# Performance work log

Measured on AMD Instinct MI355X. Metric: run time of the kernel, lower is better.

## Reference

```python
import jax, jax.numpy as jnp
import numpy as np

B, S, D = 2, 2048, 2048
H, H_KV, HD = 8, 1, 256   # attention heads, kv heads, head_dim
N_REP = H // H_KV


def setup_inputs() -> dict:
    key = jax.random.key(0)
    ks = jax.random.split(key, 8)
    std = 1.0 / np.sqrt(D)
    return {
        "hidden_states": jax.random.normal(ks[0], (B, S, D), dtype=jnp.float32),
        "attention_mask": jnp.zeros((B, 1, S, S), dtype=jnp.float32),
        "cos": jax.random.uniform(ks[1], (B, S, HD), dtype=jnp.float32),
        "sin": jax.random.uniform(ks[2], (B, S, HD), dtype=jnp.float32),
        "Wq": jax.random.normal(ks[3], (D, H * HD), dtype=jnp.float32) * std,
        "Wk": jax.random.normal(ks[4], (D, H_KV * HD), dtype=jnp.float32) * std,
        "Wv": jax.random.normal(ks[5], (D, H_KV * HD), dtype=jnp.float32) * std,
        "Wo": jax.random.normal(ks[6], (H * HD, D), dtype=jnp.float32) * std,
    }


def _rotate_half(x):
    x1, x2 = jnp.split(x, 2, axis=-1)
    return jnp.concatenate((-x2, x1), axis=-1)


def reference(hidden_states, attention_mask, cos, sin, Wq, Wk, Wv, Wo):
    b, s, _ = hidden_states.shape
    # projections -> [b, heads, s, hd]
    q = (hidden_states @ Wq).reshape(b, s, H, HD).transpose(0, 2, 1, 3)
    k = (hidden_states @ Wk).reshape(b, s, H_KV, HD).transpose(0, 2, 1, 3)
    v = (hidden_states @ Wv).reshape(b, s, H_KV, HD).transpose(0, 2, 1, 3)
    # RoPE (unsqueeze_dim=1)
    c = cos[:, None, :, :]
    sn = sin[:, None, :, :]
    q = q * c + _rotate_half(q) * sn
    k = k * c + _rotate_half(k) * sn
    # GQA: repeat kv heads
    k = jnp.repeat(k, N_REP, axis=1)
    v = jnp.repeat(v, N_REP, axis=1)
    # attention
    scores = jnp.einsum("bhqd,bhkd->bhqk", q, k) / jnp.sqrt(jnp.float32(HD))
    scores = scores + attention_mask[:, :, :, :k.shape[2]]
    attn_weights = jax.nn.softmax(scores.astype(jnp.float32), axis=-1).astype(q.dtype)
    # dropout p=0.0 -> identity
    out = jnp.einsum("bhqk,bhkd->bhqd", attn_weights, v)
    out = out.transpose(0, 2, 1, 3).reshape(b, s, H * HD)
    out = out @ Wo
    return out, attn_weights
```

## Files before the change

### kernel.cpp

```cpp
#include <hip/hip_runtime.h>
#include <hip/hip_bf16.h>

typedef float f32x4 __attribute__((ext_vector_type(4)));
typedef short short8 __attribute__((ext_vector_type(8)));
typedef unsigned int uint2v __attribute__((ext_vector_type(2)));

#define DI __device__ __forceinline__

DI unsigned short f2bf(float f) {
  unsigned int u = __float_as_uint(f);
  u += 0x7fffu + ((u >> 16) & 1u);
  return (unsigned short)(u >> 16);
}

DI unsigned int packbf(float a, float b) {
  return (unsigned int)f2bf(a) | ((unsigned int)f2bf(b) << 16);
}

DI void gload16(const unsigned short* g, unsigned short* l) {
  __builtin_amdgcn_global_load_lds((const __attribute__((address_space(1))) void*)g,
                                   (__attribute__((address_space(3))) void*)l, 16, 0, 0);
}

__global__ void cvt_bf16_kernel(const float* __restrict__ src,
                                unsigned short* __restrict__ dst, long n) {
  long i = ((long)blockIdx.x * blockDim.x + threadIdx.x) * 8;
  if (i >= n) return;
  float4 a = *(const float4*)(src + i);
  float4 b = *(const float4*)(src + i + 4);
  short8 v;
  v[0] = f2bf(a.x); v[1] = f2bf(a.y); v[2] = f2bf(a.z); v[3] = f2bf(a.w);
  v[4] = f2bf(b.x); v[5] = f2bf(b.y); v[6] = f2bf(b.z); v[7] = f2bf(b.w);
  *(short8*)(dst + i) = v;
}

__global__ void transpose_cvt_kernel(const float* __restrict__ src,
                                     unsigned short* __restrict__ dst,
                                     int ldsrc, int lddst, long sBatch, long dBatch) {
  __shared__ float tile[32][33];
  const float* s = src + (long)blockIdx.z * sBatch;
  unsigned short* d = dst + (long)blockIdx.z * dBatch;
  int c0 = blockIdx.x * 32, r0 = blockIdx.y * 32;
  int tx = threadIdx.x, ty = threadIdx.y;
#pragma unroll
  for (int k = 0; k < 4; k++)
    tile[ty + 8 * k][tx] = s[(long)(r0 + ty + 8 * k) * ldsrc + c0 + tx];
  __syncthreads();
#pragma unroll
  for (int k = 0; k < 4; k++)
    d[(long)(c0 + ty + 8 * k) * lddst + r0 + tx] = f2bf(tile[tx][ty + 8 * k]);
}

__global__ void transpose_v_kernel(const float* __restrict__ qkv,
                                   unsigned short* __restrict__ VtC) {
  __shared__ float tile[32][33];
  int b = blockIdx.z;
  int d0 = blockIdx.x * 32, s0 = blockIdx.y * 32;
  int tx = threadIdx.x, ty = threadIdx.y;
  const float* s = qkv + (long)b * 2048 * 2560 + 2304;
#pragma unroll
  for (int k = 0; k < 4; k++)
    tile[ty + 8 * k][tx] = s[(long)(s0 + ty + 8 * k) * 2560 + d0 + tx];
  __syncthreads();
  unsigned short* d = VtC + (long)b * 524288 + (long)(s0 >> 5) * 8192;
#pragma unroll
  for (int k = 0; k < 4; k++) {
    int dd = d0 + ty + 8 * k;
    d[dd * 32 + (tx ^ (((dd >> 1) & 3) << 3))] = f2bf(tile[tx][ty + 8 * k]);
  }
}

__global__ void rope_kernel(const float* __restrict__ qkv, const float* __restrict__ cs,
                            const float* __restrict__ sn, unsigned short* __restrict__ Qb,
                            unsigned short* __restrict__ Ksw) {
  int bid = blockIdx.x;
  int hp = bid % 9;
  int bs = bid / 9;
  int d = threadIdx.x;
  long row = (long)bs * 2560 + hp * 256;
  float x = qkv[row + d];
  float o = (d < 128) ? -qkv[row + d + 128] : qkv[row + d - 128];
  long ci = (long)bs * 256 + d;
  float r = x * cs[ci] + o * sn[ci];
  unsigned short v = f2bf(r);
  if (hp < 8) {
    int b = bs >> 11, s = bs & 2047;
    Qb[((long)(b * 8 + hp) * 2048 + s) * 256 + d] = v;
  } else {
    Ksw[(long)bs * 256 + (d ^ ((bs & 7) << 3))] = v;
  }
}

template <bool AF32, bool CBF16>
__launch_bounds__(256)
__global__ void gemm_bt_kernel(const void* __restrict__ Av,
                               const unsigned short* __restrict__ Btg,
                               void* __restrict__ Cv,
                               int K, int lda, int ldb, int ldc,
                               int zShift, long aBatch, long bBatch, long cBatch, long cHead) {
  __shared__ unsigned short Asm_[128 * 32];
  __shared__ unsigned short Bsm_[128 * 32];
  int z = blockIdx.z;
  int zb = z >> zShift, zh = z - (zb << zShift);
  const unsigned short* Bt = Btg + (long)zb * bBatch;
  const unsigned short* A16 = (const unsigned short*)Av + (long)z * aBatch;
  const float* A32 = (const float*)Av + (long)z * aBatch;
  int m0 = blockIdx.y * 128, n0 = blockIdx.x * 128;
  int tid = threadIdx.x, w = tid >> 6, lane = tid & 63, c = lane & 15, t = lane >> 4;
  int wm = w >> 1, wn = w & 1;
  f32x4 zero4 = {0.f, 0.f, 0.f, 0.f};
  f32x4 acc[4][4];
#pragma unroll
  for (int i = 0; i < 4; i++)
#pragma unroll
    for (int j = 0; j < 4; j++) acc[i][j] = zero4;

  for (int kt = 0; kt < K; kt += 32) {
    if constexpr (!AF32) {
#pragma unroll
      for (int jj = 0; jj < 2; jj++) {
        int slot = (w * 2 + jj) * 64 + lane;
        int r = slot >> 2, g = slot & 3;
        int gs = g ^ ((r >> 1) & 3);
        gload16(A16 + (long)(m0 + r) * lda + kt + gs * 8, Asm_ + slot * 8);
      }
    } else {
#pragma unroll
      for (int jj = 0; jj < 2; jj++) {
        int slot = jj * 256 + tid;
        int r = slot >> 2, g = slot & 3;
        int gs = g ^ ((r >> 1) & 3);
        const float* p = A32 + (long)(m0 + r) * lda + kt + gs * 8;
        float4 x = *(const float4*)p;
        float4 y = *(const float4*)(p + 4);
        short8 v;
        v[0] = f2bf(x.x); v[1] = f2bf(x.y); v[2] = f2bf(x.z); v[3] = f2bf(x.w);
        v[4] = f2bf(y.x); v[5] = f2bf(y.y); v[6] = f2bf(y.z); v[7] = f2bf(y.w);
        *(short8*)(Asm_ + slot * 8) = v;
      }
    }
#pragma unroll
    for (int jj = 0; jj < 2; jj++) {
      int slot = (w * 2 + jj) * 64 + lane;
      int r = slot >> 2, g = slot & 3;
      int gs = g ^ ((r >> 1) & 3);
      gload16(Bt + (long)(n0 + r) * ldb + kt + gs * 8, Bsm_ + slot * 8);
    }
    __syncthreads();
    short8 af[4], bfg[4];
#pragma unroll
    for (int mi = 0; mi < 4; mi++) {
      int r = wm * 64 + mi * 16 + c;
      af[mi] = *(const short8*)(Asm_ + r * 32 + ((t ^ ((r >> 1) & 3)) * 8));
    }
#pragma unroll
    for (int ni = 0; ni < 4; ni++) {
      int r = wn * 64 + ni * 16 + c;
      bfg[ni] = *(const short8*)(Bsm_ + r * 32 + ((t ^ ((r >> 1) & 3)) * 8));
    }
#pragma unroll
    for (int mi = 0; mi < 4; mi++)
#pragma unroll
      for (int ni = 0; ni < 4; ni++)
        acc[mi][ni] = __builtin_amdgcn_mfma_f32_16x16x32_bf16(af[mi], bfg[ni], acc[mi][ni], 0, 0, 0);
    __syncthreads();
  }
  long cOff = (long)zb * cBatch + zh * cHead;
#pragma unroll
  for (int mi = 0; mi < 4; mi++) {
#pragma unroll
    for (int j = 0; j < 4; j++) {
      int row = m0 + wm * 64 + mi * 16 + t * 4 + j;
#pragma unroll
      for (int ni = 0; ni < 4; ni++) {
        int col = n0 + wn * 64 + ni * 16 + c;
        float v = acc[mi][ni][j];
        long idx = cOff + (long)row * ldc + col;
        if constexpr (CBF16) ((unsigned short*)Cv)[idx] = f2bf(v);
        else ((float*)Cv)[idx] = v;
      }
    }
  }
}

#define KC 32
__launch_bounds__(512, 4)
__global__ void attn_fused_kernel(const unsigned short* __restrict__ Qb,
                                  const unsigned short* __restrict__ Ksw,
                                  const unsigned short* __restrict__ VtC,
                                  const float* __restrict__ mask,
                                  float* __restrict__ attnW,
                                  unsigned short* __restrict__ attnO) {
  __shared__ unsigned short Ksm[2][KC * 256];
  __shared__ unsigned short Vsm[2][256 * KC];
  __shared__ unsigned short Pt[4][16 * 32];
  __shared__ float red[8][16];
  const int id = blockIdx.x;
  const int sw = (id & 7) * 64 + (id >> 3);
  const int qblk = sw & 31, bh = sw >> 5;
  const int b = bh >> 3;
  const int tid = threadIdx.x, w = tid >> 6, lane = tid & 63;
  const int c = lane & 15, t = lane >> 4;
  const int s = w & 3, h = w >> 2;
  const int q0 = qblk * 64 + s * 16;
  const int kh = 16 * h;
  const float scale = 0.0625f;

  short8 qf[8];
  {
    const unsigned short* Qrow = Qb + ((long)bh * 2048 + q0 + c) * 256 + t * 8;
#pragma unroll
    for (int ks = 0; ks < 8; ks++) qf[ks] = *(const short8*)(Qrow + ks * 32);
  }

  const unsigned short* Kg = Ksw + (long)b * 524288;
  const unsigned short* Vg = VtC + (long)b * 524288;
  const float* mrow = mask + (long)b * 4194304 + (long)(q0 + c) * 2048 + kh + t * 4;

  float lp = 0.f;

#pragma unroll
  for (int i = 0; i < 2; i++) {
    int slot = i * 512 + tid;
    gload16(Kg + slot * 8, Ksm[0] + slot * 8);
  }
  for (int kc = 0; kc < 64; kc++) {
    int cur = kc & 1;
    asm volatile("s_barrier" ::: "memory");
    if (kc < 63) {
      const unsigned short* src = Kg + (long)(kc + 1) * 8192;
#pragma unroll
      for (int i = 0; i < 2; i++) {
        int slot = i * 512 + tid;
        gload16(src + slot * 8, Ksm[cur ^ 1] + slot * 8);
      }
      asm volatile("s_waitcnt vmcnt(2)" ::: "memory");
    } else {
      asm volatile("s_waitcnt vmcnt(0)" ::: "memory");
    }
    __builtin_amdgcn_sched_barrier(0);
    f32x4 mv = *(const f32x4*)(mrow + kc * 32);
    f32x4 a0 = {0.f, 0.f, 0.f, 0.f};
    __builtin_amdgcn_s_setprio(1);
#pragma unroll
    for (int ks = 0; ks < 8; ks++) {
      int g0 = ((ks * 4 + t) ^ (c & 7)) * 8;
      short8 kf = *(const short8*)(Ksm[cur] + (kh + c) * 256 + g0);
      a0 = __builtin_amdgcn_mfma_f32_16x16x32_bf16(kf, qf[ks], a0, 0, 0, 0);
    }
    __builtin_amdgcn_s_setprio(0);
#pragma unroll
    for (int j = 0; j < 4; j++) lp += __expf(a0[j] * scale + mv[j]);
  }
  lp += __shfl_xor(lp, 16);
  lp += __shfl_xor(lp, 32);
  if (t == 0) red[w][c] = lp;
  __syncthreads();
  float rinv = 1.0f / (red[s][c] + red[4 + s][c]);

  float* aWrow = attnW + (long)bh * 4194304 + (long)(q0 + c) * 2048 + kh + t * 4;
  unsigned short* myPt = &Pt[s][0];
  const int psw = ((c >> 1) & 3) << 3;
  f32x4 accO[8];
#pragma unroll
  for (int i = 0; i < 8; i++) accO[i] = (f32x4){0.f, 0.f, 0.f, 0.f};

#pragma unroll
  for (int i = 0; i < 2; i++) {
    int slot = i * 512 + tid;
    gload16(Kg + slot * 8, Ksm[0] + slot * 8);
    gload16(Vg + slot * 8, Vsm[0] + slot * 8);
  }
  for (int kc = 0; kc < 64; kc++) {
    int cur = kc & 1;
    asm volatile("s_barrier" ::: "memory");
    if (kc < 63) {
      const unsigned short* ksrc = Kg + (long)(kc + 1) * 8192;
      const unsigned short* vsrc = Vg + (long)(kc + 1) * 8192;
#pragma unroll
      for (int i = 0; i < 2; i++) {
        int slot = i * 512 + tid;
        gload16(ksrc + slot * 8, Ksm[cur ^ 1] + slot * 8);
        gload16(vsrc + slot * 8, Vsm[cur ^ 1] + slot * 8);
      }
      asm volatile("s_waitcnt vmcnt(4)" ::: "memory");
    } else {
      asm volatile("s_waitcnt vmcnt(0)" ::: "memory");
    }
    __builtin_amdgcn_sched_barrier(0);
    f32x4 mv = *(const f32x4*)(mrow + kc * 32);
    f32x4 a0 = {0.f, 0.f, 0.f, 0.f};
    __builtin_amdgcn_s_setprio(1);
#pragma unroll
    for (int ks = 0; ks < 8; ks++) {
      int g0 = ((ks * 4 + t) ^ (c & 7)) * 8;
      short8 kf = *(const short8*)(Ksm[cur] + (kh + c) * 256 + g0);
      a0 = __builtin_amdgcn_mfma_f32_16x16x32_bf16(kf, qf[ks], a0, 0, 0, 0);
    }
    __builtin_amdgcn_s_setprio(0);
    f32x4 p;
#pragma unroll
    for (int j = 0; j < 4; j++) p[j] = __expf(a0[j] * scale + mv[j]) * rinv;
    *(f32x4*)(aWrow + kc * 32) = p;
    uint2v pw;
    pw[0] = packbf(p[0], p[1]); pw[1] = packbf(p[2], p[3]);
    *(uint2v*)(myPt + c * 32 + ((kh + t * 4) ^ psw)) = pw;
    asm volatile("s_waitcnt lgkmcnt(0)" ::: "memory");
    __builtin_amdgcn_s_barrier();
    __builtin_amdgcn_sched_barrier(0);
    short8 pa = *(const short8*)(myPt + c * 32 + ((t * 8) ^ psw));
    __builtin_amdgcn_s_setprio(1);
#pragma unroll
    for (int di = 0; di < 8; di++) {
      int d = (8 * h + di) * 16 + c;
      short8 vf = *(const short8*)(Vsm[cur] + d * 32 + ((t * 8) ^ psw));
      accO[di] = __builtin_amdgcn_mfma_f32_16x16x32_bf16(pa, vf, accO[di], 0, 0, 0);
    }
    __builtin_amdgcn_s_setprio(0);
  }
  long obase = ((long)b * 2048 + q0 + t * 4) * 2048 + (bh & 7) * 256 + h * 128 + c;
#pragma unroll
  for (int di = 0; di < 8; di++)
#pragma unroll
    for (int j = 0; j < 4; j++)
      attnO[obase + (long)j * 2048 + di * 16] = f2bf(accO[di][j]);
}

extern "C" void kernel_launch(void* const* d_in, const int* in_sizes, int n_in,
                              void* d_out, int out_size, void* d_ws, size_t ws_size,
                              hipStream_t stream) {
  const float* hidden = (const float*)d_in[0];
  const float* mask = (const float*)d_in[1];
  const float* cosb = (const float*)d_in[2];
  const float* sinb = (const float*)d_in[3];
  const float* Wq = (const float*)d_in[4];
  const float* Wk = (const float*)d_in[5];
  const float* Wv = (const float*)d_in[6];
  const float* Wo = (const float*)d_in[7];
  float* out = (float*)d_out;
  float* attnW = out + 8388608;

  char* ws = (char*)d_ws;
  unsigned short* hidB  = (unsigned short*)(ws + 0);
  unsigned short* WqkvT = (unsigned short*)(ws + 16777216);
  unsigned short* WoT   = (unsigned short*)(ws + 27262976);
  float*          qkv   = (float*)(ws + 35651584);
  unsigned short* Qb    = (unsigned short*)(ws + 77594624);
  unsigned short* Ksw   = (unsigned short*)(ws + 94371840);
  unsigned short* VtC   = (unsigned short*)(ws + 96468992);
  unsigned short* attnO = (unsigned short*)(ws + 98566144);

  cvt_bf16_kernel<<<4096, 256, 0, stream>>>(hidden, hidB, 8388608L);
  transpose_cvt_kernel<<<dim3(64, 64, 1), dim3(32, 8), 0, stream>>>(Wq, WqkvT, 2048, 2048, 0, 0);
  transpose_cvt_kernel<<<dim3(8, 64, 1), dim3(32, 8), 0, stream>>>(Wk, WqkvT + (long)2048 * 2048, 256, 2048, 0, 0);
  transpose_cvt_kernel<<<dim3(8, 64, 1), dim3(32, 8), 0, stream>>>(Wv, WqkvT + (long)2304 * 2048, 256, 2048, 0, 0);
  transpose_cvt_kernel<<<dim3(64, 64, 1), dim3(32, 8), 0, stream>>>(Wo, WoT, 2048, 2048, 0, 0);
  gemm_bt_kernel<false, false><<<dim3(20, 32, 1), 256, 0, stream>>>(
      hidB, WqkvT, qkv, 2048, 2048, 2048, 2560, 0, 0, 0, 0, 0);
  rope_kernel<<<36864, 256, 0, stream>>>(qkv, cosb, sinb, Qb, Ksw);
  transpose_v_kernel<<<dim3(8, 64, 2), dim3(32, 8), 0, stream>>>(qkv, VtC);
  attn_fused_kernel<<<512, 512, 0, stream>>>(Qb, Ksw, VtC, mask, attnW, attnO);
  gemm_bt_kernel<false, false><<<dim3(16, 32, 1), 256, 0, stream>>>(
      attnO, WoT, out, 2048, 2048, 2048, 2048, 0, 0, 0, 0, 0);
}
```

Before: 395.5 us.

## Store unnormalized probabilities in pass one, reload and rescale instead of recomputing QK

The first attention pass now writes the unnormalized exp scores to the attention-weights output. The second pass reloads those values from global memory, normalizes them, and writes them back. This drops the second QK^T MFMA pass, the K tile loads and the LDS P transpose with its barrier. The cost is an extra full read and write of the fp32 attention matrix. The GEMM kernel also gets an XCD-aware block-index swizzle. The in-place rewrite relies on each element being read before it is rewritten, with the store split across the two h waves.

```diff
diff --git a/kernel.cpp b/kernel.cpp
--- a/kernel.cpp
+++ b/kernel.cpp
@@ -3,7 +3,7 @@
 
 typedef float f32x4 __attribute__((ext_vector_type(4)));
 typedef short short8 __attribute__((ext_vector_type(8)));
-typedef unsigned int uint2v __attribute__((ext_vector_type(2)));
+typedef unsigned int uint4v __attribute__((ext_vector_type(4)));
 
 #define DI __device__ __forceinline__
 
@@ -105,7 +105,11 @@
   const unsigned short* Bt = Btg + (long)zb * bBatch;
   const unsigned short* A16 = (const unsigned short*)Av + (long)z * aBatch;
   const float* A32 = (const float*)Av + (long)z * aBatch;
-  int m0 = blockIdx.y * 128, n0 = blockIdx.x * 128;
+  int nwg = gridDim.x * gridDim.y;
+  int bid = blockIdx.y * gridDim.x + blockIdx.x;
+  int qq = nwg >> 3;
+  int swz = (bid & 7) * qq + (bid >> 3);
+  int m0 = (swz / gridDim.x) * 128, n0 = (swz % gridDim.x) * 128;
   int tid = threadIdx.x, w = tid >> 6, lane = tid & 63, c = lane & 15, t = lane >> 4;
   int wm = w >> 1, wn = w & 1;
   f32x4 zero4 = {0.f, 0.f, 0.f, 0.f};
@@ -193,7 +197,6 @@
                                   unsigned short* __restrict__ attnO) {
   __shared__ unsigned short Ksm[2][KC * 256];
   __shared__ unsigned short Vsm[2][256 * KC];
-  __shared__ unsigned short Pt[4][16 * 32];
   __shared__ float red[8][16];
   const int id = blockIdx.x;
   const int sw = (id & 7) * 64 + (id >> 3);
@@ -216,6 +219,7 @@
   const unsigned short* Kg = Ksw + (long)b * 524288;
   const unsigned short* Vg = VtC + (long)b * 524288;
   const float* mrow = mask + (long)b * 4194304 + (long)(q0 + c) * 2048 + kh + t * 4;
+  float* aWrow = attnW + (long)bh * 4194304 + (long)(q0 + c) * 2048 + kh + t * 4;
 
   float lp = 0.f;
 
@@ -249,8 +253,13 @@
       a0 = __builtin_amdgcn_mfma_f32_16x16x32_bf16(kf, qf[ks], a0, 0, 0, 0);
     }
     __builtin_amdgcn_s_setprio(0);
-#pragma unroll
-    for (int j = 0; j < 4; j++) lp += __expf(a0[j] * scale + mv[j]);
+    f32x4 p;
+#pragma unroll
+    for (int j = 0; j < 4; j++) {
+      p[j] = __expf(a0[j] * scale + mv[j]);
+      lp += p[j];
+    }
+    *(f32x4*)(aWrow + kc * 32) = p;
   }
   lp += __shfl_xor(lp, 16);
   lp += __shfl_xor(lp, 32);
@@ -258,9 +267,8 @@
   __syncthreads();
   float rinv = 1.0f / (red[s][c] + red[4 + s][c]);
 
-  float* aWrow = attnW + (long)bh * 4194304 + (long)(q0 + c) * 2048 + kh + t * 4;
-  unsigned short* myPt = &Pt[s][0];
-  const int psw = ((c >> 1) & 3) << 3;
+  const float* pRow = attnW + (long)bh * 4194304 + (long)(q0 + c) * 2048 + t * 8;
+  float* sRow = attnW + (long)bh * 4194304 + (long)(q0 + c) * 2048 + t * 8;
   f32x4 accO[8];
 #pragma unroll
   for (int i = 0; i < 8; i++) accO[i] = (f32x4){0.f, 0.f, 0.f, 0.f};
@@ -268,47 +276,42 @@
 #pragma unroll
   for (int i = 0; i < 2; i++) {
     int slot = i * 512 + tid;
-    gload16(Kg + slot * 8, Ksm[0] + slot * 8);
     gload16(Vg + slot * 8, Vsm[0] + slot * 8);
   }
+  f32x4 pA = *(const f32x4*)(pRow);
+  f32x4 pB = *(const f32x4*)(pRow + 4);
   for (int kc = 0; kc < 64; kc++) {
     int cur = kc & 1;
     asm volatile("s_barrier" ::: "memory");
     if (kc < 63) {
-      const unsigned short* ksrc = Kg + (long)(kc + 1) * 8192;
       const unsigned short* vsrc = Vg + (long)(kc + 1) * 8192;
 #pragma unroll
       for (int i = 0; i < 2; i++) {
         int slot = i * 512 + tid;
-        gload16(ksrc + slot * 8, Ksm[cur ^ 1] + slot * 8);
         gload16(vsrc + slot * 8, Vsm[cur ^ 1] + slot * 8);
       }
-      asm volatile("s_waitcnt vmcnt(4)" ::: "memory");
+      asm volatile("s_waitcnt vmcnt(2)" ::: "memory");
     } else {
       asm volatile("s_waitcnt vmcnt(0)" ::: "memory");
     }
     __builtin_amdgcn_sched_barrier(0);
-    f32x4 mv = *(const f32x4*)(mrow + kc * 32);
-    f32x4 a0 = {0.f, 0.f, 0.f, 0.f};
-    __builtin_amdgcn_s_setprio(1);
-#pragma unroll
-    for (int ks = 0; ks < 8; ks++) {
-      int g0 = ((ks * 4 + t) ^ (c & 7)) * 8;
-      short8 kf = *(const short8*)(Ksm[cur] + (kh + c) * 256 + g0);
-      a0 = __builtin_amdgcn_mfma_f32_16x16x32_bf16(kf, qf[ks], a0, 0, 0, 0);
-    }
-    __builtin_amdgcn_s_setprio(0);
-    f32x4 p;
-#pragma unroll
-    for (int j = 0; j < 4; j++) p[j] = __expf(a0[j] * scale + mv[j]) * rinv;
-    *(f32x4*)(aWrow + kc * 32) = p;
-    uint2v pw;
-    pw[0] = packbf(p[0], p[1]); pw[1] = packbf(p[2], p[3]);
-    *(uint2v*)(myPt + c * 32 + ((kh + t * 4) ^ psw)) = pw;
-    asm volatile("s_waitcnt lgkmcnt(0)" ::: "memory");
-    __builtin_amdgcn_s_barrier();
-    __builtin_amdgcn_sched_barrier(0);
-    short8 pa = *(const short8*)(myPt + c * 32 + ((t * 8) ^ psw));
+    f32x4 nA, nB;
+    if (kc < 63) {
+      nA = *(const f32x4*)(pRow + (kc + 1) * 32);
+      nB = *(const f32x4*)(pRow + (kc + 1) * 32 + 4);
+    }
+    f32x4 sA, sB;
+#pragma unroll
+    for (int j = 0; j < 4; j++) { sA[j] = pA[j] * rinv; sB[j] = pB[j] * rinv; }
+    if ((t >> 1) == h) {
+      __builtin_nontemporal_store(sA, (f32x4*)(sRow + kc * 32));
+      __builtin_nontemporal_store(sB, (f32x4*)(sRow + kc * 32 + 4));
+    }
+    uint4v pu;
+    pu[0] = packbf(sA[0], sA[1]); pu[1] = packbf(sA[2], sA[3]);
+    pu[2] = packbf(sB[0], sB[1]); pu[3] = packbf(sB[2], sB[3]);
+    short8 pa = __builtin_bit_cast(short8, pu);
+    const int psw = ((c >> 1) & 3) << 3;
     __builtin_amdgcn_s_setprio(1);
 #pragma unroll
     for (int di = 0; di < 8; di++) {
@@ -317,6 +320,7 @@
       accO[di] = __builtin_amdgcn_mfma_f32_16x16x32_bf16(pa, vf, accO[di], 0, 0, 0);
     }
     __builtin_amdgcn_s_setprio(0);
+    pA = nA; pB = nB;
   }
   long obase = ((long)b * 2048 + q0 + t * 4) * 2048 + (bh & 7) * 256 + h * 128 + c;
 #pragma unroll
```

Result: slower. 513.3 us (+29.8%).

## Feed PV MFMA directly from registers, split-K reduce outputs, swizzle GEMM tiles

Applied to the files above, without the earlier changes.

The attention PV step now takes the probability fragment straight from registers as a 16x16x16 bf16 MFMA operand. This removes the LDS round trip and the per-iteration barrier that was needed to transpose P. Each wave half now covers all 256 head dims over its own half of the keys. The two halves are summed through shared memory at the end, which doubles the accumulator registers and the MFMA count per key chunk. Separately, the GEMM kernel remaps block IDs in groups of eight, likely to improve cache locality.

```diff
diff --git a/kernel.cpp b/kernel.cpp
--- a/kernel.cpp
+++ b/kernel.cpp
@@ -3,6 +3,7 @@
 
 typedef float f32x4 __attribute__((ext_vector_type(4)));
 typedef short short8 __attribute__((ext_vector_type(8)));
+typedef short short4v __attribute__((ext_vector_type(4)));
 typedef unsigned int uint2v __attribute__((ext_vector_type(2)));
 
 #define DI __device__ __forceinline__
@@ -105,7 +106,11 @@
   const unsigned short* Bt = Btg + (long)zb * bBatch;
   const unsigned short* A16 = (const unsigned short*)Av + (long)z * aBatch;
   const float* A32 = (const float*)Av + (long)z * aBatch;
-  int m0 = blockIdx.y * 128, n0 = blockIdx.x * 128;
+  int nwg = gridDim.x * gridDim.y;
+  int bid = blockIdx.y * gridDim.x + blockIdx.x;
+  int qq = nwg >> 3;
+  int swz = (bid & 7) * qq + (bid >> 3);
+  int m0 = (swz / gridDim.x) * 128, n0 = (swz % gridDim.x) * 128;
   int tid = threadIdx.x, w = tid >> 6, lane = tid & 63, c = lane & 15, t = lane >> 4;
   int wm = w >> 1, wn = w & 1;
   f32x4 zero4 = {0.f, 0.f, 0.f, 0.f};
@@ -193,7 +198,6 @@
                                   unsigned short* __restrict__ attnO) {
   __shared__ unsigned short Ksm[2][KC * 256];
   __shared__ unsigned short Vsm[2][256 * KC];
-  __shared__ unsigned short Pt[4][16 * 32];
   __shared__ float red[8][16];
   const int id = blockIdx.x;
   const int sw = (id & 7) * 64 + (id >> 3);
@@ -216,6 +220,7 @@
   const unsigned short* Kg = Ksw + (long)b * 524288;
   const unsigned short* Vg = VtC + (long)b * 524288;
   const float* mrow = mask + (long)b * 4194304 + (long)(q0 + c) * 2048 + kh + t * 4;
+  float* aWrow = attnW + (long)bh * 4194304 + (long)(q0 + c) * 2048 + kh + t * 4;
 
   float lp = 0.f;
 
@@ -258,12 +263,9 @@
   __syncthreads();
   float rinv = 1.0f / (red[s][c] + red[4 + s][c]);
 
-  float* aWrow = attnW + (long)bh * 4194304 + (long)(q0 + c) * 2048 + kh + t * 4;
-  unsigned short* myPt = &Pt[s][0];
-  const int psw = ((c >> 1) & 3) << 3;
-  f32x4 accO[8];
-#pragma unroll
-  for (int i = 0; i < 8; i++) accO[i] = (f32x4){0.f, 0.f, 0.f, 0.f};
+  f32x4 accO[16];
+#pragma unroll
+  for (int i = 0; i < 16; i++) accO[i] = (f32x4){0.f, 0.f, 0.f, 0.f};
 
 #pragma unroll
   for (int i = 0; i < 2; i++) {
@@ -271,6 +273,8 @@
     gload16(Kg + slot * 8, Ksm[0] + slot * 8);
     gload16(Vg + slot * 8, Vsm[0] + slot * 8);
   }
+  const int E0 = kh + t * 4;
+  const int g0v = E0 >> 3, o0v = E0 & 7;
   for (int kc = 0; kc < 64; kc++) {
     int cur = kc & 1;
     asm volatile("s_barrier" ::: "memory");
@@ -302,28 +306,38 @@
 #pragma unroll
     for (int j = 0; j < 4; j++) p[j] = __expf(a0[j] * scale + mv[j]) * rinv;
     *(f32x4*)(aWrow + kc * 32) = p;
-    uint2v pw;
-    pw[0] = packbf(p[0], p[1]); pw[1] = packbf(p[2], p[3]);
-    *(uint2v*)(myPt + c * 32 + ((kh + t * 4) ^ psw)) = pw;
-    asm volatile("s_waitcnt lgkmcnt(0)" ::: "memory");
-    __builtin_amdgcn_s_barrier();
-    __builtin_amdgcn_sched_barrier(0);
-    short8 pa = *(const short8*)(myPt + c * 32 + ((t * 8) ^ psw));
+    uint2v pu;
+    pu[0] = packbf(p[0], p[1]); pu[1] = packbf(p[2], p[3]);
+    short4v pa = __builtin_bit_cast(short4v, pu);
     __builtin_amdgcn_s_setprio(1);
 #pragma unroll
-    for (int di = 0; di < 8; di++) {
-      int d = (8 * h + di) * 16 + c;
-      short8 vf = *(const short8*)(Vsm[cur] + d * 32 + ((t * 8) ^ psw));
-      accO[di] = __builtin_amdgcn_mfma_f32_16x16x32_bf16(pa, vf, accO[di], 0, 0, 0);
+    for (int dt = 0; dt < 16; dt++) {
+      int d = dt * 16 + c;
+      int e = ((g0v ^ ((d >> 1) & 3)) << 3) + o0v;
+      short4v vf = *(const short4v*)(Vsm[cur] + d * 32 + e);
+      accO[dt] = __builtin_amdgcn_mfma_f32_16x16x16bf16_1k(pa, vf, accO[dt], 0, 0, 0);
     }
     __builtin_amdgcn_s_setprio(0);
   }
-  long obase = ((long)b * 2048 + q0 + t * 4) * 2048 + (bh & 7) * 256 + h * 128 + c;
-#pragma unroll
-  for (int di = 0; di < 8; di++)
-#pragma unroll
-    for (int j = 0; j < 4; j++)
-      attnO[obase + (long)j * 2048 + di * 16] = f2bf(accO[di][j]);
+  __syncthreads();
+  float* rb = ((s < 2) ? (float*)&Ksm[0][0] : (float*)&Vsm[0][0]) + (s & 1) * 4096;
+  if (h == 1) {
+#pragma unroll
+    for (int dt = 0; dt < 16; dt++)
+      *(f32x4*)(rb + dt * 256 + lane * 4) = accO[dt];
+  }
+  __syncthreads();
+  if (h == 0) {
+    long obase = ((long)b * 2048 + q0 + t * 4) * 2048 + (bh & 7) * 256 + c;
+#pragma unroll
+    for (int dt = 0; dt < 16; dt++) {
+      f32x4 o = *(const f32x4*)(rb + dt * 256 + lane * 4);
+      o += accO[dt];
+#pragma unroll
+      for (int j = 0; j < 4; j++)
+        attnO[obase + (long)j * 2048 + dt * 16] = f2bf(o[j]);
+    }
+  }
 }
 
 extern "C" void kernel_launch(void* const* d_in, const int* in_sizes, int n_in,
```

After: 463.1 us. +17.1%, slower.
